# Kernel tuning notes

Measured on AMD Instinct MI355X. Metric: run time of the kernel, lower is better.

Reference implementation:

```python
import jax, jax.numpy as jnp
import numpy as np

D = 2048
NH = 16
DH = D // NH            # 128
DHR = DH // 2           # 64
DC = D // 2             # 1024
DCQ = D // 2            # 1024
B, L = 4, 2048
ROPE_BASE = 10000.0


def setup_inputs() -> dict:
    key = jax.random.key(0)
    ks = jax.random.split(key, 10)
    s = 0.02
    inp = {
        "x": jax.random.normal(ks[0], (B, L, D), dtype=jnp.float32),
        "W_DKV": jax.random.normal(ks[1], (D, DC), dtype=jnp.float32) * s,
        "W_UK": jax.random.normal(ks[2], (DC, NH * DH), dtype=jnp.float32) * s,
        "W_UV": jax.random.normal(ks[3], (DC, NH * DH), dtype=jnp.float32) * s,
        "W_DQ": jax.random.normal(ks[4], (D, DCQ), dtype=jnp.float32) * s,
        "W_UQ": jax.random.normal(ks[5], (DCQ, NH * DH), dtype=jnp.float32) * s,
        "W_QR": jax.random.normal(ks[6], (DCQ, NH * DHR), dtype=jnp.float32) * s,
        "W_KR": jax.random.normal(ks[7], (D, DHR), dtype=jnp.float32) * s,
        "W_O": jax.random.normal(ks[8], (D, D), dtype=jnp.float32) * s,
        "s_qk": jnp.asarray(np.sqrt(DH + DHR), dtype=jnp.float32),
    }
    return inp


def _rope_tables(seq_len, dim, dtype):
    # Standard rotate-half RoPE tables: cos/sin of shape (seq_len, dim)
    inv_freq = 1.0 / (ROPE_BASE ** (jnp.arange(0, dim, 2, dtype=jnp.float32) / dim))
    t = jnp.arange(seq_len, dtype=jnp.float32)
    freqs = jnp.outer(t, inv_freq)            # (L, dim/2)
    emb = jnp.concatenate([freqs, freqs], axis=-1)  # (L, dim)
    return jnp.cos(emb).astype(dtype), jnp.sin(emb).astype(dtype)


def _apply_rope(x, cos, sin):
    # x: (B, H, L, dim); cos/sin: (L, dim)
    half = x.shape[-1] // 2
    rot = jnp.concatenate([-x[..., half:], x[..., :half]], axis=-1)
    return x * cos[None, None] + rot * sin[None, None]


def reference(x, W_DKV, W_UK, W_UV, W_DQ, W_UQ, W_QR, W_KR, W_O, s_qk):
    Bb, Ll, Dd = x.shape
    cos, sin = _rope_tables(Ll, DHR, x.dtype)

    c_kv = x @ W_DKV                                            # (B,L,DC)
    k_c = (c_kv @ W_UK).reshape(Bb, Ll, NH, DH).transpose(0, 2, 1, 3)
    v = (c_kv @ W_UV).reshape(Bb, Ll, NH, DH).transpose(0, 2, 1, 3)

    c_q = x @ W_DQ                                              # (B,L,DCQ)
    q_c = (c_q @ W_UQ).reshape(Bb, Ll, NH, DH).transpose(0, 2, 1, 3)
    q_rope = _apply_rope((c_q @ W_QR).reshape(Bb, Ll, NH, DHR).transpose(0, 2, 1, 3), cos, sin)
    k_rope = _apply_rope((x @ W_KR).reshape(Bb, Ll, 1, DHR).transpose(0, 2, 1, 3), cos, sin)
    k_rope = jnp.broadcast_to(k_rope, (Bb, NH, Ll, DHR))

    q = jnp.concatenate([q_c, q_rope], axis=-1)                 # (B,H,L,DH+DHR)
    k = jnp.concatenate([k_c, k_rope], axis=-1)

    eps = 1e-12
    q = q / jnp.maximum(jnp.linalg.norm(q, axis=-1, keepdims=True), eps)
    k = k / jnp.maximum(jnp.linalg.norm(k, axis=-1, keepdims=True), eps)

    # SDPA with scale=1.0, causal mask, q pre-scaled by s_qk
    scores = jnp.einsum("bhqd,bhkd->bhqk", q * s_qk, k)         # (B,H,L,L)
    causal = jnp.tril(jnp.ones((Ll, Ll), dtype=bool))
    scores = jnp.where(causal[None, None], scores, jnp.finfo(scores.dtype).min)
    attn = jax.nn.softmax(scores, axis=-1)
    out = jnp.einsum("bhqk,bhkd->bhqd", attn, v)                # (B,H,L,DH)
    out = out.transpose(0, 2, 1, 3).reshape(Bb, Ll, Dd)
    return out @ W_O
```

## Files before the change

### kernel.cpp

```cpp
#include <hip/hip_runtime.h>
#include <stdint.h>

typedef unsigned short u16;
typedef unsigned int u32;
typedef short bf16x8 __attribute__((ext_vector_type(8)));
typedef float f32x4 __attribute__((ext_vector_type(4)));
typedef u16 u16x4 __attribute__((ext_vector_type(4)));

#define DEV __device__ __forceinline__

DEV float bf2f(u16 u) { union { float f; u32 i; } x; x.i = ((u32)u) << 16; return x.f; }
DEV u16 f2bf(float f) {
  union { float f; u32 i; } x; x.f = f;
  u32 i = x.i;
  u32 r = (i + 0x7fffu + ((i >> 16) & 1u)) >> 16;
  return (u16)r;
}

DEV void gl_lds16(const u16* g, u16* l) {
  __builtin_amdgcn_global_load_lds((const __attribute__((address_space(1))) u32*)g,
                                   (__attribute__((address_space(3))) u32*)l, 16, 0, 0);
}

__global__ __launch_bounds__(256) void prep(const float* __restrict__ x,
                                            const float* __restrict__ W_DKV,
                                            const float* __restrict__ W_UK,
                                            const float* __restrict__ W_UV,
                                            const float* __restrict__ W_DQ,
                                            const float* __restrict__ W_UQ,
                                            const float* __restrict__ W_QR,
                                            const float* __restrict__ W_KR,
                                            const float* __restrict__ W_O,
                                            u16* __restrict__ xb,
                                            u16* __restrict__ WtDKVQ,
                                            u16* __restrict__ WtUKV,
                                            u16* __restrict__ WtO) {
  __shared__ float tile[64][65];
  const int tid = threadIdx.x;
  int bid = blockIdx.x;

  if (bid < 4096) {
#pragma unroll
    for (int it = 0; it < 4; ++it) {
      int i = bid * 1024 + it * 256 + tid;
      float4 v = ((const float4*)x)[i];
      u16x4 o;
      o.x = f2bf(v.x); o.y = f2bf(v.y); o.z = f2bf(v.z); o.w = f2bf(v.w);
      ((u16x4*)xb)[i] = o;
    }
    return;
  }
  bid -= 4096;

  const float* W; u16* Wt; int K, N;
  if (bid < 512)        { W = W_DKV; Wt = WtDKVQ;                K = 2048; N = 1024; }
  else if (bid < 1024)  { W = W_DQ;  Wt = WtDKVQ + 1024 * 2048;  K = 2048; N = 1024; bid -= 512; }
  else if (bid < 1536)  { W = W_UK;  Wt = WtUKV;                 K = 1024; N = 2048; bid -= 1024; }
  else if (bid < 2048)  { W = W_UV;  Wt = WtUKV + 2048 * 1024;   K = 1024; N = 2048; bid -= 1536; }
  else if (bid < 2560)  { W = W_UQ;  Wt = WtUKV + 4096 * 1024;   K = 1024; N = 2048; bid -= 2048; }
  else if (bid < 2816)  { W = W_QR;  Wt = WtUKV + 6144 * 1024;   K = 1024; N = 1024; bid -= 2560; }
  else if (bid < 2848)  { W = W_KR;  Wt = WtDKVQ + 2048 * 2048;  K = 2048; N = 64;   bid -= 2816; }
  else if (bid < 3040) {
    int i = (bid - 2848) * 256 + tid;
    *(uint4*)&WtDKVQ[2112 * 2048 + i * 8] = uint4{0, 0, 0, 0};
    return;
  }
  else                  { W = W_O;   Wt = WtO;                   K = 2048; N = 2048; bid -= 3040; }

  const int gx = N >> 6;
  const int n0 = (bid % gx) * 64;
  const int k0 = (bid / gx) * 64;
#pragma unroll
  for (int i = 0; i < 16; ++i) {
    int idx = tid + i * 256;
    int r = idx >> 6, c = idx & 63;
    tile[r][c] = W[(size_t)(k0 + r) * N + n0 + c];
  }
  __syncthreads();
#pragma unroll
  for (int i = 0; i < 16; ++i) {
    int idx = tid + i * 256;
    int r = idx >> 6, c = idx & 63;
    Wt[(size_t)(n0 + r) * K + k0 + c] = f2bf(tile[c][r]);
  }
}

DEV void ep_set(u16* E, int i, float v) { E[i] = f2bf(v); }
DEV void ep_set(float* E, int i, float v) { E[i] = v; }

template <typename OT, int KIND>
__global__ __launch_bounds__(512, 2) void gemm256(const u16* __restrict__ A, int lda,
                                                  const u16* __restrict__ Bt,
                                                  OT* __restrict__ C, int ldc, int K,
                                                  u16* __restrict__ X1, u16* __restrict__ X2) {
  __shared__ u16 smem[65536];
  const int tid = threadIdx.x;
  const int lane = tid & 63;
  const int w = tid >> 6;
  const int wm = w >> 2;
  const int wn = w & 3;
  const int quad = lane >> 4;
  const int l15 = lane & 15;
  const int cs = quad ^ ((l15 >> 1) & 3);
  const int nwg = gridDim.x * gridDim.y;
  const int lin = blockIdx.y * gridDim.x + blockIdx.x;
  const int swz = (lin & 7) * (nwg >> 3) + (lin >> 3);
  const int m0 = (swz / gridDim.x) * 256;
  const int n0 = (swz % gridDim.x) * 256;

  const int rloc = tid >> 2;
  const int clog = (tid & 3) ^ ((tid >> 3) & 3);
  const u16* Abase = A + ((KIND == 2 && n0 >= 4096) ? 1024 : 0);
  const size_t aoff0 = (size_t)rloc * lda + clog * 8;
  const size_t boff0 = (size_t)rloc * (size_t)K + clog * 8;
  const u16* Ag = Abase + (size_t)m0 * lda;
  const u16* Bg = Bt + (size_t)n0 * K;

  auto stageA = [&](int u, int ks2) {
    u16* dst = smem + (u & 1) * 32768 + ks2 * 8192 + w * 512;
    const u16* s0 = Ag + aoff0 + u * 64 + ks2 * 32;
    gl_lds16(s0, dst);
    gl_lds16(s0 + (size_t)128 * lda, dst + 4096);
  };
  auto stageB = [&](int u, int ks2) {
    u16* dst = smem + (u & 1) * 32768 + 16384 + ks2 * 8192 + w * 512;
    const u16* s0 = Bg + boff0 + u * 64 + ks2 * 32;
    gl_lds16(s0, dst);
    gl_lds16(s0 + (size_t)128 * (size_t)K, dst + 4096);
  };

  f32x4 acc[2][4][4] = {};
  const int nt = K >> 6;

  stageA(0, 0); stageB(0, 0); stageA(0, 1); stageB(0, 1);
  stageA(1, 0); stageB(1, 0);
  asm volatile("s_waitcnt vmcnt(4)" ::: "memory");
  __builtin_amdgcn_s_barrier();

  for (int t = 0; t < nt; ++t) {
    const u16* As_ = smem + (t & 1) * 32768;
    const u16* Bs_ = As_ + 16384;
#pragma unroll
    for (int p = 0; p < 4; ++p) {
      const int ks = p >> 1;
      const int mq = p & 1;
      const u16* Ab = As_ + ks * 8192;
      const u16* Bb = Bs_ + ks * 8192;
      bf16x8 af[4], bf[4];
#pragma unroll
      for (int mt = 0; mt < 4; ++mt)
        af[mt] = *(const bf16x8*)&Ab[(wm * 128 + mq * 64 + mt * 16 + l15) * 32 + cs * 8];
#pragma unroll
      for (int n = 0; n < 4; ++n)
        bf[n] = *(const bf16x8*)&Bb[(wn * 64 + n * 16 + l15) * 32 + cs * 8];
      if (p == 0)      { if (t + 1 < nt) stageA(t + 1, 1); }
      else if (p == 1) { if (t + 1 < nt) stageB(t + 1, 1); }
      else if (p == 2) { if (t + 2 < nt) stageA(t + 2, 0); }
      else             { if (t + 2 < nt) stageB(t + 2, 0); }
      __builtin_amdgcn_s_barrier();
      __builtin_amdgcn_s_setprio(1);
#pragma unroll
      for (int mt = 0; mt < 4; ++mt)
#pragma unroll
        for (int n = 0; n < 4; ++n)
          acc[mq][mt][n] = __builtin_amdgcn_mfma_f32_16x16x32_bf16(af[mt], bf[n], acc[mq][mt][n], 0, 0, 0);
      __builtin_amdgcn_s_setprio(0);
      if (p == 3) asm volatile("s_waitcnt vmcnt(4)" ::: "memory");
      __builtin_amdgcn_s_barrier();
    }
  }
  asm volatile("s_waitcnt vmcnt(0)" ::: "memory");
  __builtin_amdgcn_s_barrier();

  if constexpr (KIND == 2) {
    if (n0 >= 2048 && n0 < 4096) {
      u16* Ewt = smem + w * 2560;
      const int dvb = (n0 - 2048) + wn * 64;
      const int hh = dvb >> 7;
      const int dv0 = dvb & 127;
#pragma unroll
      for (int mq = 0; mq < 2; ++mq)
#pragma unroll
        for (int mh = 0; mh < 2; ++mh) {
#pragma unroll
          for (int mi = 0; mi < 2; ++mi)
#pragma unroll
            for (int n = 0; n < 4; ++n)
#pragma unroll
              for (int r = 0; r < 4; ++r)
                Ewt[(n * 16 + l15) * 40 + mi * 16 + quad * 4 + r] = f2bf(acc[mq][mh * 2 + mi][n][r]);
          asm volatile("s_waitcnt lgkmcnt(0)" ::: "memory");
          const int mbase = m0 + wm * 128 + mq * 64 + mh * 32;
          const int b_ = mbase >> 11, l_ = mbase & 2047;
          u16* dstp = X1 + ((size_t)((b_ * 16 + hh) * 128 + dv0 + lane)) * 2048 + l_;
          const u16* srcp = &Ewt[lane * 40];
#pragma unroll
          for (int k2 = 0; k2 < 4; ++k2)
            *(uint4*)&dstp[k2 * 8] = *(const uint4*)&srcp[k2 * 8];
          asm volatile("s_waitcnt lgkmcnt(0)" ::: "memory");
        }
      return;
    }
  }

  OT* Cc = C; int ldcc = ldc, col0 = n0, Nlim = 1 << 30;
  if constexpr (KIND == 1) {
    if (n0 == 2048) { Cc = (OT*)X1; ldcc = 64; col0 = 0; Nlim = 64; }
  }
  if constexpr (KIND == 2) {
    if (n0 >= 4096) { Cc = (OT*)X2; ldcc = 3072; col0 = n0 - 4096; }
  }
  OT* Ew = ((OT*)smem) + w * 1024;
#pragma unroll
  for (int mq = 0; mq < 2; ++mq) {
#pragma unroll
    for (int mt = 0; mt < 4; ++mt) {
#pragma unroll
      for (int n = 0; n < 4; ++n)
#pragma unroll
        for (int r = 0; r < 4; ++r)
          ep_set(Ew, (quad * 4 + r) * 64 + n * 16 + l15, acc[mq][mt][n][r]);
      asm volatile("s_waitcnt lgkmcnt(0)" ::: "memory");
#pragma unroll
      for (int it2 = 0; it2 < 4; ++it2) {
        int row_i = it2 * 4 + quad;
        int colg = wn * 64 + l15 * 4;
        if (colg < Nlim) {
          size_t off = (size_t)(m0 + wm * 128 + mq * 64 + mt * 16 + row_i) * ldcc + col0 + colg;
          if constexpr (sizeof(OT) == 2) {
            *(u16x4*)&Cc[off] = *(const u16x4*)&Ew[row_i * 64 + l15 * 4];
          } else {
            *(float4*)&Cc[off] = *(const float4*)&Ew[row_i * 64 + l15 * 4];
          }
        }
      }
      asm volatile("s_waitcnt lgkmcnt(0)" ::: "memory");
    }
  }
}

__global__ __launch_bounds__(256) void build_k(const u16* __restrict__ kc,
                                               const u16* __restrict__ krr,
                                               u16* __restrict__ kn) {
  const int wid = blockIdx.x * 4 + (threadIdx.x >> 6);
  const int lane = threadIdx.x & 63;
  const int token = wid >> 4;
  const int h = wid & 15;
  const int b = token >> 11;
  const int l = token & 2047;
  float v0 = bf2f(kc[(size_t)token * 2048 + h * 128 + lane]);
  float v1 = bf2f(kc[(size_t)token * 2048 + h * 128 + 64 + lane]);
  int j = lane & 31;
  float freq = __expf((float)j * -0.28782313662425574f);
  float ang = (float)l * freq;
  float cs = __cosf(ang), sn = __sinf(ang);
  float xr = bf2f(krr[(size_t)token * 64 + lane]);
  float xo = bf2f(krr[(size_t)token * 64 + (lane ^ 32)]);
  float v2 = (lane < 32) ? (xr * cs - xo * sn) : (xr * cs + xo * sn);
  float ss = v0 * v0 + v1 * v1 + v2 * v2;
#pragma unroll
  for (int off = 1; off < 64; off <<= 1) ss += __shfl_xor(ss, off, 64);
  float scale = 1.0f / fmaxf(sqrtf(ss), 1e-12f);
  u16* out = kn + (((size_t)(b * 16 + h) * 2048) + l) * 192;
  out[lane] = f2bf(v0 * scale);
  out[64 + lane] = f2bf(v1 * scale);
  out[128 + lane] = f2bf(v2 * scale);
}

__global__ __launch_bounds__(512, 2) void flash_attn(const u16* __restrict__ qcr,
                                                     const u16* __restrict__ Kn,
                                                     const u16* __restrict__ Vt,
                                                     const float* __restrict__ s_qk,
                                                     u16* __restrict__ O) {
  constexpr int L = 2048, DQK = 192, DV = 128, KVB = 64;
  constexpr int PSTR = 72;
  __shared__ u16 smem[59392];
  u16* KsBuf = smem;
  u16* VsBuf = smem + 24576;
  u16* Ps    = smem + 40960;
  const int tid = threadIdx.x;
  const int lane = tid & 63;
  const int w = tid >> 6;
  const int quad = lane >> 4;
  const int l15 = lane & 15;
  const int lin = blockIdx.x;
  const int xcd = lin & 7;
  const int g = lin >> 3;
  const int bh = ((g >> 2) << 3) | xcd;
  const int pairIdx = g & 3;
  const int b = bh >> 4, h = bh & 15;
  const float SMAX = s_qk[0];

  const u16* Kg = Kn + (size_t)bh * L * DQK;
  const u16* Vg = Vt + (size_t)bh * DV * L;

  int koffs[3], kdsts[3], voffs[2], vdsts[2];
#pragma unroll
  for (int it = 0; it < 3; ++it) {
    int p = it * 512 + w * 64 + lane;
    int r = p / 24, cp = p % 24;
    koffs[it] = r * DQK + (cp ^ (r & 7)) * 8;
    kdsts[it] = (it * 512 + w * 64) * 8;
  }
#pragma unroll
  for (int it = 0; it < 2; ++it) {
    int q = (it + 3) * 512 + w * 64 + lane - 1536;
    int dv = q >> 3, cp = q & 7;
    voffs[it] = dv * L + (cp ^ (dv & 7)) * 8;
    vdsts[it] = ((it + 3) * 512 + w * 64 - 1536) * 8;
  }

  auto stage = [&](int kt2, int bufi) {
    u16* KsB = KsBuf + bufi * 12288;
    u16* VsB = VsBuf + bufi * 8192;
    const u16* Kt = Kg + (size_t)(kt2 * KVB) * DQK;
    const u16* Vtb = Vg + kt2 * KVB;
#pragma unroll
    for (int it = 0; it < 3; ++it) gl_lds16(Kt + koffs[it], &KsB[kdsts[it]]);
#pragma unroll
    for (int it = 0; it < 2; ++it) gl_lds16(Vtb + voffs[it], &VsB[vdsts[it]]);
  };

  bf16x8 ones;
#pragma unroll
  for (int j = 0; j < 8; ++j) ones[j] = (short)0x3F80;

  for (int qp = 0; qp < 2; ++qp) {
    const int qt = (qp == 0) ? (7 - pairIdx) : pairIdx;

    bf16x8 qf[2][6];
#pragma unroll
    for (int mt = 0; mt < 2; ++mt) {
      const int row = qt * 256 + w * 32 + mt * 16 + l15;
      const u16* qr_ = qcr + (size_t)(b * 2048 + row) * 3072;
#pragma unroll
      for (int kd = 0; kd < 4; ++kd)
        qf[mt][kd] = *(const bf16x8*)&qr_[h * 128 + kd * 32 + quad * 8];
      bf16x8 a4 = *(const bf16x8*)&qr_[2048 + h * 64 + quad * 8];
      bf16x8 a5 = *(const bf16x8*)&qr_[2048 + h * 64 + 32 + quad * 8];
      float v4[8], v5[8];
      float ss = 0.f;
#pragma unroll
      for (int e = 0; e < 8; ++e) {
        int j = quad * 8 + e;
        float fr = __expf((float)j * -0.28782313662425574f);
        float ang = (float)row * fr;
        float cs2 = __cosf(ang), sn2 = __sinf(ang);
        float x4 = bf2f((u16)a4[e]), x5 = bf2f((u16)a5[e]);
        v4[e] = x4 * cs2 - x5 * sn2;
        v5[e] = x5 * cs2 + x4 * sn2;
        ss += v4[e] * v4[e] + v5[e] * v5[e];
      }
#pragma unroll
      for (int kd = 0; kd < 4; ++kd)
#pragma unroll
        for (int e = 0; e < 8; ++e) { float xv = bf2f((u16)qf[mt][kd][e]); ss += xv * xv; }
      ss += __shfl_xor(ss, 16, 64);
      ss += __shfl_xor(ss, 32, 64);
      float scale = SMAX / fmaxf(sqrtf(ss), 1e-12f);
#pragma unroll
      for (int kd = 0; kd < 4; ++kd) {
        bf16x8 t = qf[mt][kd];
#pragma unroll
        for (int e = 0; e < 8; ++e) t[e] = (short)f2bf(bf2f((u16)t[e]) * scale);
        qf[mt][kd] = t;
      }
      bf16x8 t4, t5;
#pragma unroll
      for (int e = 0; e < 8; ++e) { t4[e] = (short)f2bf(v4[e] * scale); t5[e] = (short)f2bf(v5[e] * scale); }
      qf[mt][4] = t4; qf[mt][5] = t5;
    }

    f32x4 oacc[2][8] = {};
    f32x4 accL[2] = {};

    const int nkv = 4 * (qt + 1);
    stage(0, 0);
    __syncthreads();

    for (int kt = 0; kt < nkv; ++kt) {
      const int cur = kt & 1;
      if (kt + 1 < nkv) stage(kt + 1, cur ^ 1);
      const u16* KsC = KsBuf + cur * 12288;
      const u16* VsC = VsBuf + cur * 8192;

      f32x4 s[2][4] = {};
      __builtin_amdgcn_s_setprio(1);
#pragma unroll
      for (int kd = 0; kd < 6; ++kd) {
#pragma unroll
        for (int nt = 0; nt < 4; ++nt) {
          int row = nt * 16 + l15;
          int cp = (kd * 4 + quad) ^ (l15 & 7);
          bf16x8 bb = *(const bf16x8*)&KsC[row * DQK + cp * 8];
#pragma unroll
          for (int mt = 0; mt < 2; ++mt)
            s[mt][nt] = __builtin_amdgcn_mfma_f32_16x16x32_bf16(qf[mt][kd], bb, s[mt][nt], 0, 0, 0);
        }
      }
      __builtin_amdgcn_s_setprio(0);

      const int kcol0 = kt * KVB + l15;
      u16* Pw = &Ps[w * 32 * PSTR];
#pragma unroll
      for (int mt = 0; mt < 2; ++mt) {
        const int qrow_base = qt * 256 + w * 32 + mt * 16 + quad * 4;
#pragma unroll
        for (int r = 0; r < 4; ++r)
#pragma unroll
          for (int nt = 0; nt < 4; ++nt) {
            float p = (kcol0 + nt * 16 > qrow_base + r) ? 0.f : __expf(s[mt][nt][r] - SMAX);
            Pw[(mt * 16 + quad * 4 + r) * PSTR + nt * 16 + l15] = f2bf(p);
          }
      }
      asm volatile("s_waitcnt lgkmcnt(0)" ::: "memory");

      __builtin_amdgcn_s_setprio(1);
      bf16x8 pf[2][2];
#pragma unroll
      for (int mt = 0; mt < 2; ++mt)
#pragma unroll
        for (int kc2 = 0; kc2 < 2; ++kc2) {
          pf[mt][kc2] = *(const bf16x8*)&Pw[(mt * 16 + l15) * PSTR + kc2 * 32 + quad * 8];
          accL[mt] = __builtin_amdgcn_mfma_f32_16x16x32_bf16(pf[mt][kc2], ones, accL[mt], 0, 0, 0);
        }
#pragma unroll
      for (int nt2 = 0; nt2 < 8; ++nt2) {
        const int dv = nt2 * 16 + l15;
#pragma unroll
        for (int kc2 = 0; kc2 < 2; ++kc2) {
          int lc = (kc2 * 4 + quad) ^ (l15 & 7);
          bf16x8 vv = *(const bf16x8*)&VsC[dv * KVB + lc * 8];
#pragma unroll
          for (int mt = 0; mt < 2; ++mt)
            oacc[mt][nt2] = __builtin_amdgcn_mfma_f32_16x16x32_bf16(pf[mt][kc2], vv, oacc[mt][nt2], 0, 0, 0);
        }
      }
      __builtin_amdgcn_s_setprio(0);
      __syncthreads();
    }

    float rinv[2][4];
#pragma unroll
    for (int mt = 0; mt < 2; ++mt)
#pragma unroll
      for (int r = 0; r < 4; ++r) rinv[mt][r] = 1.0f / accL[mt][r];
    u16* Ew = smem + w * 2048;
#pragma unroll
    for (int mt = 0; mt < 2; ++mt) {
#pragma unroll
      for (int nt2 = 0; nt2 < 8; ++nt2)
#pragma unroll
        for (int r = 0; r < 4; ++r)
          Ew[(quad * 4 + r) * 128 + nt2 * 16 + l15] = f2bf(oacc[mt][nt2][r] * rinv[mt][r]);
      asm volatile("s_waitcnt lgkmcnt(0)" ::: "memory");
#pragma unroll
      for (int it2 = 0; it2 < 4; ++it2) {
        int row_i = it2 * 4 + quad;
        int lg = qt * 256 + w * 32 + mt * 16 + row_i;
        uint4 v = *(const uint4*)&Ew[row_i * 128 + l15 * 8];
        *(uint4*)&O[((size_t)b * L + lg) * 2048 + h * 128 + l15 * 8] = v;
      }
      asm volatile("s_waitcnt lgkmcnt(0)" ::: "memory");
    }
    __syncthreads();
  }
}

extern "C" void kernel_launch(void* const* d_in, const int* in_sizes, int n_in,
                              void* d_out, int out_size, void* d_ws, size_t ws_size,
                              hipStream_t stream) {
  const float* x     = (const float*)d_in[0];
  const float* W_DKV = (const float*)d_in[1];
  const float* W_UK  = (const float*)d_in[2];
  const float* W_UV  = (const float*)d_in[3];
  const float* W_DQ  = (const float*)d_in[4];
  const float* W_UQ  = (const float*)d_in[5];
  const float* W_QR  = (const float*)d_in[6];
  const float* W_KR  = (const float*)d_in[7];
  const float* W_O   = (const float*)d_in[8];
  const float* s_qk  = (const float*)d_in[9];

  char* base = (char*)d_ws;
  u16* xb     = (u16*)(base);
  u16* WtDKVQ = (u16*)(base + (size_t)33554432);
  u16* WtUKV  = (u16*)(base + (size_t)42991616);
  u16* WtO    = (u16*)(base + (size_t)57671680);
  u16* ckvq   = (u16*)(base + (size_t)66060288);
  u16* kc     = (u16*)(base + (size_t)99614720);
  u16* Vt     = (u16*)(base + (size_t)133169152);
  u16* qcr    = (u16*)(base + (size_t)166723584);
  u16* kr     = (u16*)(base + (size_t)217055232);
  u16* kn = (u16*)(base);
  u16* O  = ckvq;

  prep<<<8160, 256, 0, stream>>>(x, W_DKV, W_UK, W_UV, W_DQ, W_UQ, W_QR, W_KR, W_O,
                                 xb, WtDKVQ, WtUKV, WtO);

  gemm256<u16, 1><<<dim3(9, 32), 512, 0, stream>>>(xb, 2048, WtDKVQ, ckvq, 2048, 2048, kr, nullptr);

  gemm256<u16, 2><<<dim3(28, 32), 512, 0, stream>>>(ckvq, 2048, WtUKV, kc, 2048, 1024, Vt, qcr);

  build_k<<<32768, 256, 0, stream>>>(kc, kr, kn);

  flash_attn<<<dim3(256), 512, 0, stream>>>(qcr, kn, Vt, s_qk, O);

  gemm256<float, 0><<<dim3(8, 32), 512, 0, stream>>>(O, 2048, WtO, (float*)d_out, 2048, 2048,
                                                     nullptr, nullptr);
}
```

Measured before the change: 623.1 us.

## Move narrow x@W_KR GEMM into up-projection kernel tail and regroup tile order

The 64-column x@W_KR projection was previously padded to a full 256-wide N tile in the first GEMM, which added a ninth column of mostly wasted work. It now runs as 32 extra slim workgroups appended to the second GEMM launch, each with its own small double-buffered MFMA loop. The tile-to-workgroup mapping is also regrouped into 4-row M groups per XCD for better L2 reuse. The cost is load imbalance, since the slim blocks run a 32-step K loop with low MFMA density next to the full tiles.

Result: faster. 587.5 us (-5.7%).

```diff
diff --git a/kernel.cpp b/kernel.cpp
--- a/kernel.cpp
+++ b/kernel.cpp
@@ -34,6 +34,7 @@
                                             u16* __restrict__ xb,
                                             u16* __restrict__ WtDKVQ,
                                             u16* __restrict__ WtUKV,
+                                            u16* __restrict__ WtKR,
                                             u16* __restrict__ WtO) {
   __shared__ float tile[64][65];
   const int tid = threadIdx.x;
@@ -59,13 +60,8 @@
   else if (bid < 2048)  { W = W_UV;  Wt = WtUKV + 2048 * 1024;   K = 1024; N = 2048; bid -= 1536; }
   else if (bid < 2560)  { W = W_UQ;  Wt = WtUKV + 4096 * 1024;   K = 1024; N = 2048; bid -= 2048; }
   else if (bid < 2816)  { W = W_QR;  Wt = WtUKV + 6144 * 1024;   K = 1024; N = 1024; bid -= 2560; }
-  else if (bid < 2848)  { W = W_KR;  Wt = WtDKVQ + 2048 * 2048;  K = 2048; N = 64;   bid -= 2816; }
-  else if (bid < 3040) {
-    int i = (bid - 2848) * 256 + tid;
-    *(uint4*)&WtDKVQ[2112 * 2048 + i * 8] = uint4{0, 0, 0, 0};
-    return;
-  }
-  else                  { W = W_O;   Wt = WtO;                   K = 2048; N = 2048; bid -= 3040; }
+  else if (bid < 2848)  { W = W_KR;  Wt = WtKR;                  K = 2048; N = 64;   bid -= 2816; }
+  else                  { W = W_O;   Wt = WtO;                   K = 2048; N = 2048; bid -= 2848; }
 
   const int gx = N >> 6;
   const int n0 = (bid % gx) * 64;
@@ -92,7 +88,10 @@
 __global__ __launch_bounds__(512, 2) void gemm256(const u16* __restrict__ A, int lda,
                                                   const u16* __restrict__ Bt,
                                                   OT* __restrict__ C, int ldc, int K,
-                                                  u16* __restrict__ X1, u16* __restrict__ X2) {
+                                                  u16* __restrict__ X1, u16* __restrict__ X2,
+                                                  const u16* __restrict__ A2,
+                                                  const u16* __restrict__ B2,
+                                                  u16* __restrict__ C2) {
   __shared__ u16 smem[65536];
   const int tid = threadIdx.x;
   const int lane = tid & 63;
@@ -102,11 +101,80 @@
   const int quad = lane >> 4;
   const int l15 = lane & 15;
   const int cs = quad ^ ((l15 >> 1) & 3);
-  const int nwg = gridDim.x * gridDim.y;
-  const int lin = blockIdx.y * gridDim.x + blockIdx.x;
-  const int swz = (lin & 7) * (nwg >> 3) + (lin >> 3);
-  const int m0 = (swz / gridDim.x) * 256;
-  const int n0 = (swz % gridDim.x) * 256;
+
+  int m0, n0;
+  if constexpr (KIND == 2) {
+    const int lin2 = blockIdx.x;
+    const int xcd2 = lin2 & 7;
+    const int pos = lin2 >> 3;
+    if (pos >= 112) {
+      const int idx = xcd2 * 4 + (pos - 112);
+      u16* Ab2 = smem;
+      u16* Bb2 = smem + 32768;
+      const u16* Ag2 = A2 + (size_t)(idx * 256) * 2048;
+      auto stg = [&](int t2, int bufi) {
+        u16* Ad = Ab2 + bufi * 16384;
+        u16* Bd = Bb2 + bufi * 4096;
+#pragma unroll
+        for (int i = 0; i < 4; ++i) {
+          int cb = i * 512 + w * 64;
+          int c = cb + lane;
+          int r = c >> 3, cp = (c & 7) ^ (r & 7);
+          gl_lds16(Ag2 + (size_t)r * 2048 + t2 * 64 + cp * 8, &Ad[cb * 8]);
+        }
+        {
+          int cb = w * 64;
+          int c = cb + lane;
+          int r = c >> 3, cp = (c & 7) ^ (r & 7);
+          gl_lds16(B2 + (size_t)r * 2048 + t2 * 64 + cp * 8, &Bd[cb * 8]);
+        }
+      };
+      f32x4 acc2[2][4] = {};
+      stg(0, 0);
+      __syncthreads();
+      for (int t2 = 0; t2 < 32; ++t2) {
+        int cur = t2 & 1;
+        if (t2 + 1 < 32) stg(t2 + 1, cur ^ 1);
+        const u16* Ad = Ab2 + cur * 16384;
+        const u16* Bd = Bb2 + cur * 4096;
+#pragma unroll
+        for (int kq = 0; kq < 2; ++kq) {
+          bf16x8 bfr[4];
+#pragma unroll
+          for (int n = 0; n < 4; ++n)
+            bfr[n] = *(const bf16x8*)&Bd[(n * 16 + l15) * 64 + ((kq * 4 + quad) ^ (l15 & 7)) * 8];
+#pragma unroll
+          for (int mt = 0; mt < 2; ++mt) {
+            bf16x8 afr = *(const bf16x8*)&Ad[(w * 32 + mt * 16 + l15) * 64 + ((kq * 4 + quad) ^ (l15 & 7)) * 8];
+#pragma unroll
+            for (int n = 0; n < 4; ++n)
+              acc2[mt][n] = __builtin_amdgcn_mfma_f32_16x16x32_bf16(afr, bfr[n], acc2[mt][n], 0, 0, 0);
+          }
+        }
+        __syncthreads();
+      }
+#pragma unroll
+      for (int mt = 0; mt < 2; ++mt)
+#pragma unroll
+        for (int n = 0; n < 4; ++n)
+#pragma unroll
+          for (int r = 0; r < 4; ++r)
+            C2[(size_t)(idx * 256 + w * 32 + mt * 16 + quad * 4 + r) * 64 + n * 16 + l15] =
+                f2bf(acc2[mt][n][r]);
+      return;
+    }
+    const int c = xcd2 * 112 + pos;
+    const int g4 = c >> 2;
+    n0 = (g4 % 28) * 256;
+    m0 = ((g4 / 28) * 4 + (c & 3)) * 256;
+  } else {
+    const int nwg = gridDim.x * gridDim.y;
+    const int lin = blockIdx.y * gridDim.x + blockIdx.x;
+    const int swz = (lin & 7) * (nwg >> 3) + (lin >> 3);
+    const int g4 = swz >> 2;
+    n0 = (g4 % gridDim.x) * 256;
+    m0 = ((g4 / gridDim.x) * 4 + (swz & 3)) * 256;
+  }
 
   const int rloc = tid >> 2;
   const int clog = (tid & 3) ^ ((tid >> 3) & 3);
@@ -203,10 +271,7 @@
     }
   }
 
-  OT* Cc = C; int ldcc = ldc, col0 = n0, Nlim = 1 << 30;
-  if constexpr (KIND == 1) {
-    if (n0 == 2048) { Cc = (OT*)X1; ldcc = 64; col0 = 0; Nlim = 64; }
-  }
+  OT* Cc = C; int ldcc = ldc, col0 = n0;
   if constexpr (KIND == 2) {
     if (n0 >= 4096) { Cc = (OT*)X2; ldcc = 3072; col0 = n0 - 4096; }
   }
@@ -224,14 +289,11 @@
 #pragma unroll
       for (int it2 = 0; it2 < 4; ++it2) {
         int row_i = it2 * 4 + quad;
-        int colg = wn * 64 + l15 * 4;
-        if (colg < Nlim) {
-          size_t off = (size_t)(m0 + wm * 128 + mq * 64 + mt * 16 + row_i) * ldcc + col0 + colg;
-          if constexpr (sizeof(OT) == 2) {
-            *(u16x4*)&Cc[off] = *(const u16x4*)&Ew[row_i * 64 + l15 * 4];
-          } else {
-            *(float4*)&Cc[off] = *(const float4*)&Ew[row_i * 64 + l15 * 4];
-          }
+        size_t off = (size_t)(m0 + wm * 128 + mq * 64 + mt * 16 + row_i) * ldcc + col0 + wn * 64 + l15 * 4;
+        if constexpr (sizeof(OT) == 2) {
+          *(u16x4*)&Cc[off] = *(const u16x4*)&Ew[row_i * 64 + l15 * 4];
+        } else {
+          *(float4*)&Cc[off] = *(const float4*)&Ew[row_i * 64 + l15 * 4];
         }
       }
       asm volatile("s_waitcnt lgkmcnt(0)" ::: "memory");
@@ -272,7 +334,8 @@
                                                      const u16* __restrict__ Vt,
                                                      const float* __restrict__ s_qk,
                                                      u16* __restrict__ O) {
-  constexpr int L = 2048, DQK = 192, DV = 128, KVB = 64;
+  constexpr int L = 2048, DQK = 192, KVB = 64;
+  constexpr int DV = 128; (void)DV;
   constexpr int PSTR = 72;
   __shared__ u16 smem[59392];
   u16* KsBuf = smem;
@@ -292,7 +355,7 @@
   const float SMAX = s_qk[0];
 
   const u16* Kg = Kn + (size_t)bh * L * DQK;
-  const u16* Vg = Vt + (size_t)bh * DV * L;
+  const u16* Vg = Vt + (size_t)bh * 128 * L;
 
   int koffs[3], kdsts[3], voffs[2], vdsts[2];
 #pragma unroll
@@ -491,20 +554,23 @@
   u16* Vt     = (u16*)(base + (size_t)133169152);
   u16* qcr    = (u16*)(base + (size_t)166723584);
   u16* kr     = (u16*)(base + (size_t)217055232);
+  u16* WtKR   = (u16*)(base + (size_t)218103808);
   u16* kn = (u16*)(base);
   u16* O  = ckvq;
 
-  prep<<<8160, 256, 0, stream>>>(x, W_DKV, W_UK, W_UV, W_DQ, W_UQ, W_QR, W_KR, W_O,
-                                 xb, WtDKVQ, WtUKV, WtO);
-
-  gemm256<u16, 1><<<dim3(9, 32), 512, 0, stream>>>(xb, 2048, WtDKVQ, ckvq, 2048, 2048, kr, nullptr);
-
-  gemm256<u16, 2><<<dim3(28, 32), 512, 0, stream>>>(ckvq, 2048, WtUKV, kc, 2048, 1024, Vt, qcr);
+  prep<<<7968, 256, 0, stream>>>(x, W_DKV, W_UK, W_UV, W_DQ, W_UQ, W_QR, W_KR, W_O,
+                                 xb, WtDKVQ, WtUKV, WtKR, WtO);
+
+  gemm256<u16, 0><<<dim3(8, 32), 512, 0, stream>>>(xb, 2048, WtDKVQ, ckvq, 2048, 2048,
+                                                   nullptr, nullptr, nullptr, nullptr, nullptr);
+
+  gemm256<u16, 2><<<dim3(928), 512, 0, stream>>>(ckvq, 2048, WtUKV, kc, 2048, 1024,
+                                                 Vt, qcr, xb, WtKR, kr);
 
   build_k<<<32768, 256, 0, stream>>>(kc, kr, kn);
 
   flash_attn<<<dim3(256), 512, 0, stream>>>(qcr, kn, Vt, s_qk, O);
 
   gemm256<float, 0><<<dim3(8, 32), 512, 0, stream>>>(O, 2048, WtO, (float*)d_out, 2048, 2048,
-                                                     nullptr, nullptr);
-}
+                                                     nullptr, nullptr, nullptr, nullptr, nullptr);
+}
```
